# Performance work log

Measured on AMD Instinct MI355X. Metric: run time of the kernel, lower is better.

The kernel has to match this reference:

```python
import jax, jax.numpy as jnp
import numpy as np


def _conv(x, w, pad):
    # NCHW conv, stride 1, symmetric padding
    return jax.lax.conv_general_dilated(
        x, w, window_strides=(1, 1), padding=[(pad, pad), (pad, pad)],
        dimension_numbers=("NCHW", "OIHW", "NCHW"))


def setup_inputs() -> dict:
    key = jax.random.key(0)
    ks = jax.random.split(key, 8)
    B, L_I, L_H, L_Q, IM, N_ACT = 64, 2, 150, 10, 128, 5
    return {
        "input_view": jax.random.normal(ks[0], (B, L_I, IM, IM), jnp.float32),
        "state_x": jax.random.randint(ks[1], (B,), 0, IM),
        "state_y": jax.random.randint(ks[2], (B,), 0, IM),
        "k": 50,
        "h_w": jax.random.normal(ks[3], (L_H, L_I, 3, 3), jnp.float32) * 0.05,
        "h_b": jnp.zeros((L_H,), jnp.float32),
        "r_w": jax.random.normal(ks[4], (1, L_H, 1, 1), jnp.float32) * 0.05,
        "q_w": jax.random.normal(ks[5], (L_Q, 1, 3, 3), jnp.float32) * 0.1,
        "w": jax.random.normal(ks[6], (L_Q, 1, 3, 3), jnp.float32) * 0.1,
        "fc_w": jax.random.normal(ks[7], (N_ACT, L_Q), jnp.float32) * 0.1,
    }


def reference(input_view, state_x, state_y, k, h_w, h_b, r_w, q_w, w, fc_w):
    # process_input: h -> r -> q -> v
    h = _conv(input_view, h_w, 1) + h_b[None, :, None, None]   # (B, l_h, H, W)
    r = _conv(h, r_w, 0)                                        # (B, 1,  H, W)
    q = _conv(r, q_w, 1)                                        # (B, l_q, H, W)
    v = jnp.max(q, axis=1, keepdims=True)                       # (B, 1,  H, W)

    # value_iteration: k-1 updates of v, then final q
    wq = jnp.concatenate([q_w, w], axis=1)                      # (l_q, 2, 3, 3)

    def body(v, _):
        qi = _conv(jnp.concatenate([r, v], axis=1), wq, 1)
        return jnp.max(qi, axis=1, keepdims=True), None

    v, _ = jax.lax.scan(body, v, None, length=k - 1)
    q = _conv(jnp.concatenate([r, v], axis=1), wq, 1)           # (B, l_q, H, W)

    # get_action: gather q at agent states, project to action logits
    B = q.shape[0]
    q_out = q[jnp.arange(B), :, state_x, state_y]               # (B, l_q)
    logits = q_out @ fc_w.T                                     # (B, 5)
    return logits
```

## Files before the change

### kernel.cpp

```cpp
#include <hip/hip_runtime.h>


#define IM 128
#define Bn 64
#define LQ 10
#define LH 150
#define NACT 5
#define TW 136
#define NTHR 1024

#define RV 26
#define NRQ 51

__global__ __launch_bounds__(NTHR) void prep_r(
    const float* __restrict__ in, const float* __restrict__ h_w,
    const float* __restrict__ h_b, const float* __restrict__ r_w,
    const float* __restrict__ q_w, float* __restrict__ rglob,
    float* __restrict__ v0g) {
    __shared__ float in_t[2][36][IM];
    __shared__ float r_loc[34][TW];
    __shared__ float wbuf[19];

    const int bid = blockIdx.x;
    const int b   = bid >> 2;
    const int y0  = (bid & 3) * 32;
    const int tid = threadIdx.x;
    const float* inb = in + ((size_t)b * 2 << 14);

    if (tid < 18) {
        float s = 0.f;
        for (int c = 0; c < LH; ++c) s = fmaf(r_w[c], h_w[c * 18 + tid], s);
        wbuf[tid] = s;
    } else if (tid == 18) {
        float s = 0.f;
        for (int c = 0; c < LH; ++c) s = fmaf(r_w[c], h_b[c], s);
        wbuf[18] = s;
    }

    for (int i = tid; i < 2 * 36 * 32; i += NTHR) {
        int ch = i / (36 * 32);
        int rest = i - ch * (36 * 32);
        int ir = rest >> 5, x4 = (rest & 31) * 4;
        int yi = y0 - 2 + ir;
        float4 v = make_float4(0.f, 0.f, 0.f, 0.f);
        if (yi >= 0 && yi < IM) v = *(const float4*)&inb[(ch << 14) + (yi << 7) + x4];
        *(float4*)&in_t[ch][ir][x4] = v;
    }
    __syncthreads();

    for (int i = tid; i < 34 * IM; i += NTHR) {
        int rr = i >> 7, x = i & 127;
        int yr = y0 - 1 + rr;
        float acc = 0.f;
        if (yr >= 0 && yr < IM) {
            acc = wbuf[18];
#pragma unroll
            for (int ch = 0; ch < 2; ++ch)
#pragma unroll
                for (int dy = 0; dy < 3; ++dy) {
                    const float* row = &in_t[ch][rr + dy][0];
                    float l = (x > 0) ? row[x - 1] : 0.f;
                    float m = row[x];
                    float r2 = (x < IM - 1) ? row[x + 1] : 0.f;
                    acc = fmaf(wbuf[ch * 9 + dy * 3 + 0], l,
                          fmaf(wbuf[ch * 9 + dy * 3 + 1], m,
                          fmaf(wbuf[ch * 9 + dy * 3 + 2], r2, acc)));
                }
        }
        r_loc[rr][x + 4] = acc;
    }
    if (tid < 34) { r_loc[tid][3] = 0.f; r_loc[tid][132] = 0.f; }
    __syncthreads();

    float* rg = rglob + ((size_t)b << 14);
    for (int i = tid; i < 32 * IM; i += NTHR) {
        int rr = 1 + (i >> 7), x = i & 127;
        rg[((y0 + (i >> 7)) << 7) + x] = r_loc[rr][x + 4];
    }
    float* vg = v0g + ((size_t)b << 14);
    for (int i = tid; i < 32 * IM; i += NTHR) {
        int vr = i >> 7, x = i & 127;
        float nv = -3.4e38f;
#pragma unroll
        for (int a = 0; a < LQ; ++a) {
            float acc = 0.f;
#pragma unroll
            for (int dy = 0; dy < 3; ++dy)
#pragma unroll
                for (int dx = 0; dx < 3; ++dx)
                    acc = fmaf(q_w[a * 9 + dy * 3 + dx], r_loc[vr + dy][x + 3 + dx], acc);
            nv = fmaxf(nv, acc);
        }
        vg[((y0 + vr) << 7) + x] = nv;
    }
}

__device__ __forceinline__ float act9(const float* __restrict__ wt, float rqv,
                                      const float (&win)[8][3], int i) {
    float acc = rqv;
    acc = fmaf(wt[0], win[i][0],     acc);
    acc = fmaf(wt[1], win[i][1],     acc);
    acc = fmaf(wt[2], win[i][2],     acc);
    acc = fmaf(wt[3], win[i + 1][0], acc);
    acc = fmaf(wt[4], win[i + 1][1], acc);
    acc = fmaf(wt[5], win[i + 1][2], acc);
    acc = fmaf(wt[6], win[i + 2][0], acc);
    acc = fmaf(wt[7], win[i + 2][1], acc);
    acc = fmaf(wt[8], win[i + 2][2], acc);
    return acc;
}

__device__ __forceinline__ void vi_step(
    const float (&vin)[50][TW], float (&vout)[50][TW],
    const float (&rq)[6][LQ], const float* __restrict__ w,
    int base, int c, int y0, int lo, int hi)
{
    __syncthreads();
    float win[8][3];
#pragma unroll
    for (int r = 0; r < 8; ++r) {
        win[r][0] = vin[base - 1 + r][c + 3];
        win[r][1] = vin[base - 1 + r][c + 4];
        win[r][2] = vin[base - 1 + r][c + 5];
    }
#pragma unroll
    for (int i = 0; i < 6; ++i) {
        const int tr = base + i;
        if (tr >= lo && tr <= hi) {
            float a0 = act9(w + 0 * 9, rq[i][0], win, i);
            float a1 = act9(w + 1 * 9, rq[i][1], win, i);
            float a2 = act9(w + 2 * 9, rq[i][2], win, i);
            float g0 = fmaxf(fmaxf(a0, a1), a2);
            float a3 = act9(w + 3 * 9, rq[i][3], win, i);
            float a4 = act9(w + 4 * 9, rq[i][4], win, i);
            float a5 = act9(w + 5 * 9, rq[i][5], win, i);
            float g1 = fmaxf(fmaxf(a3, a4), a5);
            float a6 = act9(w + 6 * 9, rq[i][6], win, i);
            float a7 = act9(w + 7 * 9, rq[i][7], win, i);
            float a8 = act9(w + 8 * 9, rq[i][8], win, i);
            float g2 = fmaxf(fmaxf(a6, a7), a8);
            float a9 = act9(w + 9 * 9, rq[i][9], win, i);
            float nv = fmaxf(fmaxf(fmaxf(g0, g1), g2), a9);
            int yv = y0 + tr - 9;
            vout[tr][c + 4] = (yv >= 0 && yv < IM) ? nv : 0.f;
        }
    }
}

__global__ __launch_bounds__(NTHR) void vin_tb(
    const float* __restrict__ rglob, const float* __restrict__ q_w,
    const float* __restrict__ w, const float* __restrict__ vin_g,
    float* __restrict__ vout_g)
{
    __shared__ float v_t[2][50][TW];
    __shared__ float r_t[50][TW];

    const int bid  = blockIdx.x;
    const int b    = bid >> 2;
    const int y0   = (bid & 3) * 32;
    const int tid  = threadIdx.x;
    const int c    = tid & 127;
    const int k    = tid >> 7;
    const int base = 1 + 6 * k;

    const float* rg = rglob + ((size_t)b << 14);
    for (int i = tid; i < 50 * 32; i += NTHR) {
        int rr = i >> 5, x4 = (i & 31) * 4;
        int yr = y0 - 9 + rr;
        float4 v = make_float4(0.f, 0.f, 0.f, 0.f);
        if (yr >= 0 && yr < IM) v = *(const float4*)&rg[(yr << 7) + x4];
        *(float4*)&r_t[rr][x4 + 4] = v;
    }
    if (tid < 50) { r_t[tid][3] = 0.f; r_t[tid][132] = 0.f; }

    const float* vb = vin_g + ((size_t)b << 14);
    for (int i = tid; i < 48 * 32; i += NTHR) {
        int tr = 1 + (i >> 5), x4 = (i & 31) * 4;
        int yv = y0 + tr - 9;
        float4 v = make_float4(0.f, 0.f, 0.f, 0.f);
        if (yv >= 0 && yv < IM) v = *(const float4*)&vb[(yv << 7) + x4];
        *(float4*)&v_t[0][tr][x4 + 4] = v;
    }
    if (tid < TW) {
        v_t[0][0][tid] = 0.f; v_t[0][49][tid] = 0.f;
        v_t[1][0][tid] = 0.f; v_t[1][49][tid] = 0.f;
    }
    if (tid < 50) {
        v_t[0][tid][3] = 0.f; v_t[0][tid][132] = 0.f;
        v_t[1][tid][3] = 0.f; v_t[1][tid][132] = 0.f;
    }
    __syncthreads();

    float rq[6][LQ];
    {
        float win[8][3];
#pragma unroll
        for (int r = 0; r < 8; ++r) {
            win[r][0] = r_t[base - 1 + r][c + 3];
            win[r][1] = r_t[base - 1 + r][c + 4];
            win[r][2] = r_t[base - 1 + r][c + 5];
        }
#pragma unroll
        for (int a = 0; a < LQ; ++a)
#pragma unroll
            for (int i = 0; i < 6; ++i)
                rq[i][a] = act9(q_w + a * 9, 0.f, win, i);
    }

#pragma unroll 1
    for (int t = 1; t <= 8; t += 2) {
        vi_step(v_t[0], v_t[1], rq, w, base, c, y0, 1 + t, 48 - t);
        vi_step(v_t[1], v_t[0], rq, w, base, c, y0, 2 + t, 47 - t);
    }
    __syncthreads();

    float* vo = vout_g + ((size_t)b << 14);
#pragma unroll
    for (int i = 0; i < 6; ++i) {
        int tr = base + i;
        if (tr >= 9 && tr <= 40) {
            int yv = y0 + tr - 9;
            vo[(yv << 7) + c] = v_t[0][tr][c + 4];
        }
    }
}

__global__ __launch_bounds__(NTHR) void cone_finish(
    const float* __restrict__ rglob, const float* __restrict__ q_w,
    const float* __restrict__ w, const float* __restrict__ v24g,
    const int* __restrict__ sx, const int* __restrict__ sy,
    const float* __restrict__ fc_w, float* __restrict__ out)
{
    __shared__ float v_c[2][2 * RV + 1][2 * RV + 2];
    __shared__ float rq_c[NRQ][NRQ][11];

    const int b   = blockIdx.x;
    const int tid = threadIdx.x;
    const int Y   = sx[b];
    const int X   = sy[b];

    const float* vg = v24g + ((size_t)b << 14);
    for (int p = tid; p < (2 * RV + 1) * (2 * RV + 1); p += NTHR) {
        int i = p / (2 * RV + 1), j = p - i * (2 * RV + 1);
        int iy = Y - RV + i, ix = X - RV + j;
        v_c[0][i][j] = (iy >= 0 && iy < IM && ix >= 0 && ix < IM) ? vg[(iy << 7) + ix] : 0.f;
    }

    const float* rg = rglob + ((size_t)b << 14);
    for (int p = tid; p < NRQ * NRQ; p += NTHR) {
        int i2 = p / NRQ, j2 = p - i2 * NRQ;
        int cy = Y - 25 + i2, cx = X - 25 + j2;
        float rv[3][3];
#pragma unroll
        for (int dy = 0; dy < 3; ++dy)
#pragma unroll
            for (int dx = 0; dx < 3; ++dx) {
                int iy = cy + dy - 1, ix = cx + dx - 1;
                rv[dy][dx] = (iy >= 0 && iy < IM && ix >= 0 && ix < IM)
                             ? rg[(iy << 7) + ix] : 0.f;
            }
#pragma unroll
        for (int a = 0; a < LQ; ++a) {
            const float* qt = q_w + a * 9;
            float acc = 0.f;
#pragma unroll
            for (int dy = 0; dy < 3; ++dy)
#pragma unroll
                for (int dx = 0; dx < 3; ++dx)
                    acc = fmaf(qt[dy * 3 + dx], rv[dy][dx], acc);
            rq_c[i2][j2][a] = acc;
        }
    }

    int par = 0;
    const int rr0 = tid >> 6, cc = tid & 63;
#pragma unroll 1
    for (int t = 25; t <= 49; ++t) {
        const int rho = 50 - t;
        const int W   = 2 * rho + 1;
        const int off = RV - rho;
        __syncthreads();
        const float (*vp)[2 * RV + 2] = v_c[par];
        float (*vo)[2 * RV + 2] = v_c[par ^ 1];
        for (int rr = rr0; rr < W; rr += 16) {
            if (cc < W) {
                int lr = off + rr, lc = off + cc;
                float v00 = vp[lr - 1][lc - 1], v01 = vp[lr - 1][lc], v02 = vp[lr - 1][lc + 1];
                float v10 = vp[lr    ][lc - 1], v11 = vp[lr    ][lc], v12 = vp[lr    ][lc + 1];
                float v20 = vp[lr + 1][lc - 1], v21 = vp[lr + 1][lc], v22 = vp[lr + 1][lc + 1];
                const float* rqp = &rq_c[lr - 1][lc - 1][0];
                float nv = -3.4e38f;
#pragma unroll
                for (int a = 0; a < LQ; ++a) {
                    const float* wt = w + a * 9;
                    float acc = rqp[a];
                    acc = fmaf(wt[0], v00, acc); acc = fmaf(wt[1], v01, acc);
                    acc = fmaf(wt[2], v02, acc); acc = fmaf(wt[3], v10, acc);
                    acc = fmaf(wt[4], v11, acc); acc = fmaf(wt[5], v12, acc);
                    acc = fmaf(wt[6], v20, acc); acc = fmaf(wt[7], v21, acc);
                    acc = fmaf(wt[8], v22, acc);
                    nv = fmaxf(nv, acc);
                }
                int iy = Y - RV + lr, ix = X - RV + lc;
                vo[lr][lc] = (iy >= 0 && iy < IM && ix >= 0 && ix < IM) ? nv : 0.f;
            }
        }
        par ^= 1;
    }
    __syncthreads();

    if (tid < NACT) {
        const float (*vf)[2 * RV + 2] = v_c[par];
        float s = 0.f;
#pragma unroll
        for (int a = 0; a < LQ; ++a) {
            const float* wt = w + a * 9;
            float acc = rq_c[RV - 1][RV - 1][a];
#pragma unroll
            for (int dy = 0; dy < 3; ++dy)
#pragma unroll
                for (int dx = 0; dx < 3; ++dx)
                    acc = fmaf(wt[dy * 3 + dx], vf[RV - 1 + dy][RV - 1 + dx], acc);
            s = fmaf(acc, fc_w[tid * LQ + a], s);
        }
        out[b * NACT + tid] = s;
    }
}

extern "C" void kernel_launch(void* const* d_in, const int* in_sizes, int n_in,
                              void* d_out, int out_size, void* d_ws, size_t ws_size,
                              hipStream_t stream) {
    const float* input = (const float*)d_in[0];
    const int*   sx    = (const int*)d_in[1];
    const int*   sy    = (const int*)d_in[2];
    const float* h_w   = (const float*)d_in[4];
    const float* h_b   = (const float*)d_in[5];
    const float* r_w   = (const float*)d_in[6];
    const float* q_w   = (const float*)d_in[7];
    const float* w     = (const float*)d_in[8];
    const float* fc_w  = (const float*)d_in[9];
    float* out = (float*)d_out;

    char* ws = (char*)d_ws;
    float* vgA   = (float*)ws;
    float* vgB   = (float*)(ws + (4u << 20));
    float* rglob = (float*)(ws + (8u << 20));

    prep_r<<<Bn * 4, NTHR, 0, stream>>>(input, h_w, h_b, r_w, q_w, rglob, vgA);

    vin_tb<<<Bn * 4, NTHR, 0, stream>>>(rglob, q_w, w, vgA, vgB);
    vin_tb<<<Bn * 4, NTHR, 0, stream>>>(rglob, q_w, w, vgB, vgA);
    vin_tb<<<Bn * 4, NTHR, 0, stream>>>(rglob, q_w, w, vgA, vgB);

    cone_finish<<<Bn, NTHR, 0, stream>>>(rglob, q_w, w, vgB, sx, sy, fc_w, out);
}
```

Measured before the change: 181.4 us.

## Restrict value-iteration passes to row bands around agent's state row

Each value-iteration pass now computes only a band of rows centred on the agent's row (sx), and the band narrows with each pass (88, 72, 56 rows) instead of the full 128-row image. This is possible because the final gather needs only the dependency cone of the agent position. The kernel is templated on band ownership and rows per thread, which shrinks shared memory and register tiles. The cone_finish kernel also stages r into shared memory once instead of doing nine guarded global loads per point. The risk is correctness at band edges: rows outside each band are never rewritten, so later passes depend on the shrinking bands still covering every row the final cone reads.

```diff
diff --git a/kernel.cpp b/kernel.cpp
--- a/kernel.cpp
+++ b/kernel.cpp
@@ -95,8 +95,9 @@
     }
 }
 
+template<int WR>
 __device__ __forceinline__ float act9(const float* __restrict__ wt, float rqv,
-                                      const float (&win)[8][3], int i) {
+                                      const float (&win)[WR][3], int i) {
     float acc = rqv;
     acc = fmaf(wt[0], win[i][0],     acc);
     acc = fmaf(wt[1], win[i][1],     acc);
@@ -110,116 +111,116 @@
     return acc;
 }
 
-__device__ __forceinline__ void vi_step(
-    const float (&vin)[50][TW], float (&vout)[50][TW],
-    const float (&rq)[6][LQ], const float* __restrict__ w,
-    int base, int c, int y0, int lo, int hi)
-{
-    __syncthreads();
-    float win[8][3];
-#pragma unroll
-    for (int r = 0; r < 8; ++r) {
-        win[r][0] = vin[base - 1 + r][c + 3];
-        win[r][1] = vin[base - 1 + r][c + 4];
-        win[r][2] = vin[base - 1 + r][c + 5];
-    }
-#pragma unroll
-    for (int i = 0; i < 6; ++i) {
-        const int tr = base + i;
-        if (tr >= lo && tr <= hi) {
-            float a0 = act9(w + 0 * 9, rq[i][0], win, i);
-            float a1 = act9(w + 1 * 9, rq[i][1], win, i);
-            float a2 = act9(w + 2 * 9, rq[i][2], win, i);
-            float g0 = fmaxf(fmaxf(a0, a1), a2);
-            float a3 = act9(w + 3 * 9, rq[i][3], win, i);
-            float a4 = act9(w + 4 * 9, rq[i][4], win, i);
-            float a5 = act9(w + 5 * 9, rq[i][5], win, i);
-            float g1 = fmaxf(fmaxf(a3, a4), a5);
-            float a6 = act9(w + 6 * 9, rq[i][6], win, i);
-            float a7 = act9(w + 7 * 9, rq[i][7], win, i);
-            float a8 = act9(w + 8 * 9, rq[i][8], win, i);
-            float g2 = fmaxf(fmaxf(a6, a7), a8);
-            float a9 = act9(w + 9 * 9, rq[i][9], win, i);
-            float nv = fmaxf(fmaxf(fmaxf(g0, g1), g2), a9);
-            int yv = y0 + tr - 9;
-            vout[tr][c + 4] = (yv >= 0 && yv < IM) ? nv : 0.f;
-        }
-    }
-}
-
-__global__ __launch_bounds__(NTHR) void vin_tb(
+template<int OWN, int SR>
+__global__ __launch_bounds__(NTHR) void vin_band(
     const float* __restrict__ rglob, const float* __restrict__ q_w,
     const float* __restrict__ w, const float* __restrict__ vin_g,
-    float* __restrict__ vout_g)
+    float* __restrict__ vout_g, const int* __restrict__ sx)
 {
-    __shared__ float v_t[2][50][TW];
-    __shared__ float r_t[50][TW];
+    constexpr int DATA = OWN + 16;
+    constexpr int ROWS = 8 * SR + 3;
+    __shared__ float v_t[2][ROWS][TW];
+    __shared__ float r_t[ROWS][TW];
 
     const int bid  = blockIdx.x;
     const int b    = bid >> 2;
-    const int y0   = (bid & 3) * 32;
     const int tid  = threadIdx.x;
     const int c    = tid & 127;
     const int k    = tid >> 7;
-    const int base = 1 + 6 * k;
+    const int base_k = 1 + SR * k;
+
+    const int Y = sx[b];
+    int base = Y - 2 * OWN;
+    if (base < 0) base = 0;
+    if (base > IM - 4 * OWN) base = IM - 4 * OWN;
+    const int o = base + OWN * (bid & 3);
 
     const float* rg = rglob + ((size_t)b << 14);
-    for (int i = tid; i < 50 * 32; i += NTHR) {
+    for (int i = tid; i < (DATA + 2) * 32; i += NTHR) {
         int rr = i >> 5, x4 = (i & 31) * 4;
-        int yr = y0 - 9 + rr;
+        int yr = o - 9 + rr;
         float4 v = make_float4(0.f, 0.f, 0.f, 0.f);
         if (yr >= 0 && yr < IM) v = *(const float4*)&rg[(yr << 7) + x4];
         *(float4*)&r_t[rr][x4 + 4] = v;
     }
-    if (tid < 50) { r_t[tid][3] = 0.f; r_t[tid][132] = 0.f; }
+    if (tid < ROWS) { r_t[tid][3] = 0.f; r_t[tid][132] = 0.f; }
 
     const float* vb = vin_g + ((size_t)b << 14);
-    for (int i = tid; i < 48 * 32; i += NTHR) {
+    for (int i = tid; i < DATA * 32; i += NTHR) {
         int tr = 1 + (i >> 5), x4 = (i & 31) * 4;
-        int yv = y0 + tr - 9;
+        int yv = o + tr - 9;
         float4 v = make_float4(0.f, 0.f, 0.f, 0.f);
         if (yv >= 0 && yv < IM) v = *(const float4*)&vb[(yv << 7) + x4];
         *(float4*)&v_t[0][tr][x4 + 4] = v;
     }
-    if (tid < TW) {
-        v_t[0][0][tid] = 0.f; v_t[0][49][tid] = 0.f;
-        v_t[1][0][tid] = 0.f; v_t[1][49][tid] = 0.f;
-    }
-    if (tid < 50) {
+    if (tid < TW) { v_t[0][0][tid] = 0.f; v_t[1][0][tid] = 0.f; }
+    if (tid < ROWS) {
         v_t[0][tid][3] = 0.f; v_t[0][tid][132] = 0.f;
         v_t[1][tid][3] = 0.f; v_t[1][tid][132] = 0.f;
     }
     __syncthreads();
 
-    float rq[6][LQ];
+    float rq[SR][LQ];
     {
-        float win[8][3];
-#pragma unroll
-        for (int r = 0; r < 8; ++r) {
-            win[r][0] = r_t[base - 1 + r][c + 3];
-            win[r][1] = r_t[base - 1 + r][c + 4];
-            win[r][2] = r_t[base - 1 + r][c + 5];
+        float win[SR + 2][3];
+#pragma unroll
+        for (int r = 0; r < SR + 2; ++r) {
+            win[r][0] = r_t[base_k - 1 + r][c + 3];
+            win[r][1] = r_t[base_k - 1 + r][c + 4];
+            win[r][2] = r_t[base_k - 1 + r][c + 5];
         }
 #pragma unroll
         for (int a = 0; a < LQ; ++a)
 #pragma unroll
-            for (int i = 0; i < 6; ++i)
-                rq[i][a] = act9(q_w + a * 9, 0.f, win, i);
+            for (int i = 0; i < SR; ++i)
+                rq[i][a] = act9<SR + 2>(q_w + a * 9, 0.f, win, i);
     }
 
 #pragma unroll 1
-    for (int t = 1; t <= 8; t += 2) {
-        vi_step(v_t[0], v_t[1], rq, w, base, c, y0, 1 + t, 48 - t);
-        vi_step(v_t[1], v_t[0], rq, w, base, c, y0, 2 + t, 47 - t);
+    for (int t = 1; t <= 8; ++t) {
+        const int p = (t - 1) & 1;
+        const float (*vin)[TW] = v_t[p];
+        float (*vout)[TW] = v_t[p ^ 1];
+        const int lo = 1 + t, hi = DATA - t;
+        __syncthreads();
+        float win[SR + 2][3];
+#pragma unroll
+        for (int r = 0; r < SR + 2; ++r) {
+            win[r][0] = vin[base_k - 1 + r][c + 3];
+            win[r][1] = vin[base_k - 1 + r][c + 4];
+            win[r][2] = vin[base_k - 1 + r][c + 5];
+        }
+#pragma unroll
+        for (int i = 0; i < SR; ++i) {
+            const int tr = base_k + i;
+            if (tr >= lo && tr <= hi) {
+                float a0 = act9<SR + 2>(w + 0 * 9, rq[i][0], win, i);
+                float a1 = act9<SR + 2>(w + 1 * 9, rq[i][1], win, i);
+                float a2 = act9<SR + 2>(w + 2 * 9, rq[i][2], win, i);
+                float g0 = fmaxf(fmaxf(a0, a1), a2);
+                float a3 = act9<SR + 2>(w + 3 * 9, rq[i][3], win, i);
+                float a4 = act9<SR + 2>(w + 4 * 9, rq[i][4], win, i);
+                float a5 = act9<SR + 2>(w + 5 * 9, rq[i][5], win, i);
+                float g1 = fmaxf(fmaxf(a3, a4), a5);
+                float a6 = act9<SR + 2>(w + 6 * 9, rq[i][6], win, i);
+                float a7 = act9<SR + 2>(w + 7 * 9, rq[i][7], win, i);
+                float a8 = act9<SR + 2>(w + 8 * 9, rq[i][8], win, i);
+                float g2 = fmaxf(fmaxf(a6, a7), a8);
+                float a9 = act9<SR + 2>(w + 9 * 9, rq[i][9], win, i);
+                float nv = fmaxf(fmaxf(fmaxf(g0, g1), g2), a9);
+                int yv = o + tr - 9;
+                vout[tr][c + 4] = (yv >= 0 && yv < IM) ? nv : 0.f;
+            }
+        }
     }
     __syncthreads();
 
     float* vo = vout_g + ((size_t)b << 14);
 #pragma unroll
-    for (int i = 0; i < 6; ++i) {
-        int tr = base + i;
-        if (tr >= 9 && tr <= 40) {
-            int yv = y0 + tr - 9;
+    for (int i = 0; i < SR; ++i) {
+        int tr = base_k + i;
+        if (tr >= 9 && tr <= OWN + 8) {
+            int yv = o + tr - 9;
             vo[(yv << 7) + c] = v_t[0][tr][c + 4];
         }
     }
@@ -233,6 +234,7 @@
 {
     __shared__ float v_c[2][2 * RV + 1][2 * RV + 2];
     __shared__ float rq_c[NRQ][NRQ][11];
+    __shared__ float r_c[2 * RV + 1][2 * RV + 4];
 
     const int b   = blockIdx.x;
     const int tid = threadIdx.x;
@@ -240,25 +242,18 @@
     const int X   = sy[b];
 
     const float* vg = v24g + ((size_t)b << 14);
+    const float* rg = rglob + ((size_t)b << 14);
     for (int p = tid; p < (2 * RV + 1) * (2 * RV + 1); p += NTHR) {
         int i = p / (2 * RV + 1), j = p - i * (2 * RV + 1);
         int iy = Y - RV + i, ix = X - RV + j;
-        v_c[0][i][j] = (iy >= 0 && iy < IM && ix >= 0 && ix < IM) ? vg[(iy << 7) + ix] : 0.f;
-    }
-
-    const float* rg = rglob + ((size_t)b << 14);
+        bool in = (iy >= 0 && iy < IM && ix >= 0 && ix < IM);
+        v_c[0][i][j] = in ? vg[(iy << 7) + ix] : 0.f;
+        r_c[i][j]    = in ? rg[(iy << 7) + ix] : 0.f;
+    }
+    __syncthreads();
+
     for (int p = tid; p < NRQ * NRQ; p += NTHR) {
         int i2 = p / NRQ, j2 = p - i2 * NRQ;
-        int cy = Y - 25 + i2, cx = X - 25 + j2;
-        float rv[3][3];
-#pragma unroll
-        for (int dy = 0; dy < 3; ++dy)
-#pragma unroll
-            for (int dx = 0; dx < 3; ++dx) {
-                int iy = cy + dy - 1, ix = cx + dx - 1;
-                rv[dy][dx] = (iy >= 0 && iy < IM && ix >= 0 && ix < IM)
-                             ? rg[(iy << 7) + ix] : 0.f;
-            }
 #pragma unroll
         for (int a = 0; a < LQ; ++a) {
             const float* qt = q_w + a * 9;
@@ -267,7 +262,7 @@
             for (int dy = 0; dy < 3; ++dy)
 #pragma unroll
                 for (int dx = 0; dx < 3; ++dx)
-                    acc = fmaf(qt[dy * 3 + dx], rv[dy][dx], acc);
+                    acc = fmaf(qt[dy * 3 + dx], r_c[i2 + dy][j2 + dx], acc);
             rq_c[i2][j2][a] = acc;
         }
     }
@@ -348,9 +343,9 @@
 
     prep_r<<<Bn * 4, NTHR, 0, stream>>>(input, h_w, h_b, r_w, q_w, rglob, vgA);
 
-    vin_tb<<<Bn * 4, NTHR, 0, stream>>>(rglob, q_w, w, vgA, vgB);
-    vin_tb<<<Bn * 4, NTHR, 0, stream>>>(rglob, q_w, w, vgB, vgA);
-    vin_tb<<<Bn * 4, NTHR, 0, stream>>>(rglob, q_w, w, vgA, vgB);
+    vin_band<22, 5><<<Bn * 4, NTHR, 0, stream>>>(rglob, q_w, w, vgA, vgB, sx);
+    vin_band<18, 5><<<Bn * 4, NTHR, 0, stream>>>(rglob, q_w, w, vgB, vgA, sx);
+    vin_band<14, 4><<<Bn * 4, NTHR, 0, stream>>>(rglob, q_w, w, vgA, vgB, sx);
 
     cone_finish<<<Bn, NTHR, 0, stream>>>(rglob, q_w, w, vgB, sx, sy, fc_w, out);
 }
```

Measured after the change: 153.0 us. -15.7%, faster.
